# Performance work log

Measured on AMD Instinct MI355X. Metric: run time of the kernel, lower is better.

## Reference

```python
import jax, jax.numpy as jnp
import numpy as np

B, S, HID, NH = 2, 2048, 1024, 16
HD = HID // NH  # head_dim = 64


def setup_inputs() -> dict:
    key = jax.random.key(0)
    ks = jax.random.split(key, 11)
    sc = 1.0 / np.sqrt(HID)
    inp = {
        "query": jax.random.normal(ks[0], (B, S, HID), jnp.float32),
        "key_": jax.random.normal(ks[1], (B, S, HID), jnp.float32),
        "value": jax.random.normal(ks[2], (B, S, HID), jnp.float32),
        "Wq": jax.random.normal(ks[3], (HID, HID), jnp.float32) * sc,
        "bq": jnp.zeros((HID,), jnp.float32),
        "Wk": jax.random.normal(ks[4], (HID, HID), jnp.float32) * sc,
        "bk": jnp.zeros((HID,), jnp.float32),
        "Wv": jax.random.normal(ks[5], (HID, HID), jnp.float32) * sc,
        "bv": jnp.zeros((HID,), jnp.float32),
        "Wo": jax.random.normal(ks[6], (HID, HID), jnp.float32) * sc,
        "bo": jnp.zeros((HID,), jnp.float32),
    }
    return inp


def _split_heads(x):
    # [B, S, HID] -> [B, NH, S, HD]
    return x.reshape(B, S, NH, HD).transpose(0, 2, 1, 3)


def reference(query, key_, value, Wq, bq, Wk, bk, Wv, bv, Wo, bo):
    q = _split_heads(query @ Wq + bq)
    k = _split_heads(key_ @ Wk + bk)
    v = _split_heads(value @ Wv + bv)
    scale = 1.0 / jnp.sqrt(jnp.asarray(HD, q.dtype))
    # [B, NH, S, S] scores (unfused attention, as in the original module)
    scores = jnp.einsum("bhqd,bhkd->bhqk", q, k) * scale
    attn = jax.nn.softmax(scores, axis=-1)
    ctx = jnp.einsum("bhqk,bhkd->bhqd", attn, v)  # [B, NH, S, HD]
    ctx = ctx.transpose(0, 2, 1, 3).reshape(B, S, HID)
    return ctx @ Wo + bo
```

## Files before the change

kernel.cpp:

```cpp
#include <hip/hip_runtime.h>


typedef unsigned short u16;
typedef unsigned int u32;
typedef __bf16 bf16x8 __attribute__((ext_vector_type(8)));
typedef float f32x4 __attribute__((ext_vector_type(4)));
typedef u16 u16x4 __attribute__((ext_vector_type(4)));

__device__ __forceinline__ u16 f2bf(float f) {
  __bf16 h = (__bf16)f;
  return *(u16*)&h;
}

__device__ __forceinline__ void gll16(const void* g, void* l) {
  __builtin_amdgcn_global_load_lds(
      (const __attribute__((address_space(1))) u32*)g,
      (__attribute__((address_space(3))) u32*)l, 16, 0, 0);
}

__global__ __launch_bounds__(256) void prep_kernel(
    const float* __restrict__ q32, const float* __restrict__ k32,
    const float* __restrict__ v32,
    u16* __restrict__ qb, u16* __restrict__ kb, u16* __restrict__ vb,
    const float* __restrict__ W0, const float* __restrict__ W1,
    const float* __restrict__ W2, const float* __restrict__ W3,
    u16* __restrict__ T0, u16* __restrict__ T1,
    u16* __restrict__ T2, u16* __restrict__ T3) {
  int blk = blockIdx.x, tid = threadIdx.x;
  if (blk < 12288) {
    int which = blk >> 12;
    const float* in = (which == 0) ? q32 : (which == 1) ? k32 : v32;
    u16* out = (which == 0) ? qb : (which == 1) ? kb : vb;
    int i = (blk & 4095) * 256 + tid;
    float4 v = ((const float4*)in)[i];
    u16x4 o;
    o.x = f2bf(v.x); o.y = f2bf(v.y); o.z = f2bf(v.z); o.w = f2bf(v.w);
    ((u16x4*)out)[i] = o;
  } else {
    int tb = blk - 12288;
    int z = tb >> 10, rest = tb & 1023;
    const float* W = (z == 0) ? W0 : (z == 1) ? W1 : (z == 2) ? W2 : W3;
    u16* WT = (z == 0) ? T0 : (z == 1) ? T1 : (z == 2) ? T2 : T3;
    __shared__ float t[32][33];
    int bx = (rest & 31) * 32, by = (rest >> 5) * 32;
    int tx = tid & 31, ty = tid >> 5;
#pragma unroll
    for (int i = ty; i < 32; i += 8) t[i][tx] = W[(by + i) * 1024 + bx + tx];
    __syncthreads();
#pragma unroll
    for (int i = ty; i < 32; i += 8) WT[(bx + i) * 1024 + by + tx] = f2bf(t[tx][i]);
  }
}

struct GemmJob {
  const u16* A; const u16* BT; const float* bias;
  float* Cf; u16* Cb; int mode; float oscale;
};

template <int BN>
__global__ __launch_bounds__(256, 4) void gemm_sbuf(GemmJob j0, GemmJob j1, GemmJob j2) {
  constexpr int NT = BN / 32;
  constexpr int NBC = BN / 32;
  const int K = 1024, N = 1024;
  __shared__ __align__(16) u16 As[128 * 64];
  __shared__ __align__(16) u16 Bs[BN * 64];
  int blk = blockIdx.x, tid = threadIdx.x;
  int z, r0, bm, bn;
  if (BN == 128) {
    z = blk >> 8; r0 = blk & 255;
    int xcd = r0 & 7, i5 = r0 >> 3;
    bm = (xcd * 4 + (i5 & 3)) * 128;
    bn = (i5 >> 2) * 128;
  } else {
    z = 0; r0 = blk;
    int xcd = r0 & 7, i6 = r0 >> 3;
    bm = (xcd * 4 + (i6 & 3)) * 128;
    bn = (i6 >> 2) * 64;
  }
  GemmJob j = (z == 0) ? j0 : (z == 1) ? j1 : j2;
  int w = tid >> 6, lane = tid & 63, quad = lane >> 4, l16 = lane & 15;
  int wr = (w >> 1) * 64, wc = (w & 1) * (BN / 2);
  f32x4 acc[4][NT] = {};

  auto stage = [&](int kk) {
#pragma unroll
    for (int i = 0; i < 4; ++i) {
      int c = tid + i * 256;
      int r = c >> 3, jp = c & 7, jg = jp ^ (r & 7);
      gll16(&j.A[(size_t)(bm + r) * K + kk + jg * 8], &As[c * 8]);
    }
#pragma unroll
    for (int i = 0; i < NBC; ++i) {
      int c = tid + i * 256;
      int r = c >> 3, jp = c & 7, jg = jp ^ (r & 7);
      gll16(&j.BT[(size_t)(bn + r) * K + kk + jg * 8], &Bs[c * 8]);
    }
  };

  for (int it = 0; it < 16; ++it) {
    __syncthreads();
    stage(it * 64);
    __syncthreads();
#pragma unroll
    for (int ks = 0; ks < 2; ++ks) {
      bf16x8 af[4], bfr[NT];
#pragma unroll
      for (int mt = 0; mt < 4; ++mt) {
        int row = wr + mt * 16 + l16;
        af[mt] = *(const bf16x8*)&As[row * 64 + (((ks * 4 + quad) ^ (row & 7))) * 8];
      }
#pragma unroll
      for (int nt = 0; nt < NT; ++nt) {
        int row = wc + nt * 16 + l16;
        bfr[nt] = *(const bf16x8*)&Bs[row * 64 + (((ks * 4 + quad) ^ (row & 7))) * 8];
      }
#pragma unroll
      for (int mt = 0; mt < 4; ++mt)
#pragma unroll
        for (int nt = 0; nt < NT; ++nt)
          acc[mt][nt] = __builtin_amdgcn_mfma_f32_16x16x32_bf16(af[mt], bfr[nt], acc[mt][nt], 0, 0, 0);
    }
  }

#pragma unroll
  for (int mt = 0; mt < 4; ++mt)
#pragma unroll
    for (int nt = 0; nt < NT; ++nt)
#pragma unroll
      for (int r = 0; r < 4; ++r) {
        int row = bm + wr + mt * 16 + quad * 4 + r;
        int col = bn + wc + nt * 16 + l16;
        float v = (acc[mt][nt][r] + j.bias[col]) * j.oscale;
        if (j.mode == 0) {
          j.Cf[(size_t)row * N + col] = v;
        } else {
          int b = row >> 11, s = row & 2047, h = col >> 6, d = col & 63;
          u16 bv = f2bf(v);
          if (j.mode == 1)
            j.Cb[(((size_t)(b * 16 + h) * 2048 + s) << 6) + d] = bv;
          else
            j.Cb[((size_t)(b * 16 + h) * 64 + d) * 2048 + s] = bv;
        }
      }
}

__global__ __launch_bounds__(512) void attn_kernel(
    const u16* __restrict__ Q,
    const u16* __restrict__ Kk,
    const u16* __restrict__ VT,
    u16* __restrict__ ctx)
{
  __shared__ __align__(16) u16 Ks[128 * 64];
  __shared__ __align__(16) u16 Vs[64 * 128];
  __shared__ __align__(16) u16 PT[8 * 16 * 128];

  int blk = blockIdx.x;
  int qt = (blk >> 3) & 15;
  int bh = (blk & 7) * 4 + (blk >> 7);
  int b = bh >> 4, h = bh & 15;
  const u16* Qb = Q + ((size_t)bh * 2048 + qt * 128) * 64;
  const u16* Kb = Kk + (size_t)bh * 2048 * 64;
  const u16* Vb = VT + (size_t)bh * 64 * 2048;
  int tid = threadIdx.x, w = tid >> 6, lane = tid & 63, quad = lane >> 4, l16 = lane & 15;
  int rowbase = w * 16;
  u16* PTw = &PT[w * 16 * 128];

  bf16x8 qf[2];
#pragma unroll
  for (int ks = 0; ks < 2; ++ks)
    qf[ks] = *(const bf16x8*)&Qb[(rowbase + l16) * 64 + ks * 32 + quad * 8];

  f32x4 Oacc[4] = {};
  float lacc = 0.f;

  for (int kv = 0; kv < 16; ++kv) {
    int kbase = kv * 128;
    __syncthreads();
#pragma unroll
    for (int i = 0; i < 2; ++i) {
      int c = tid + i * 512;
      int r = c >> 3, jp = c & 7, jg = jp ^ (r & 7);
      gll16(&Kb[(size_t)(kbase + r) * 64 + jg * 8], &Ks[c * 8]);
    }
#pragma unroll
    for (int i = 0; i < 2; ++i) {
      int c = tid + i * 512;
      int d = c >> 4, jp = c & 15, jg = jp ^ (d & 15);
      gll16(&Vb[(size_t)d * 2048 + kbase + jg * 8], &Vs[c * 8]);
    }
    __syncthreads();

    f32x4 Sacc[8] = {};
#pragma unroll
    for (int nt = 0; nt < 8; ++nt) {
      int r = nt * 16 + l16;
#pragma unroll
      for (int ks = 0; ks < 2; ++ks) {
        bf16x8 kfr = *(const bf16x8*)&Ks[r * 64 + ((ks * 4 + quad) ^ (l16 & 7)) * 8];
        Sacc[nt] = __builtin_amdgcn_mfma_f32_16x16x32_bf16(kfr, qf[ks], Sacc[nt], 0, 0, 0);
      }
    }

#pragma unroll
    for (int nt = 0; nt < 8; ++nt) {
      u16x4 pk;
#pragma unroll
      for (int r = 0; r < 4; ++r) {
        float p = exp2f(Sacc[nt][r]);
        lacc += p;
        pk[r] = f2bf(p);
      }
      int jj = nt * 2 + (quad >> 1);
      *(u16x4*)&PTw[l16 * 128 + ((jj ^ l16) * 8) + (quad & 1) * 4] = pk;
    }

#pragma unroll
    for (int ks2 = 0; ks2 < 4; ++ks2) {
      bf16x8 pfB = *(const bf16x8*)&PTw[l16 * 128 + (((ks2 * 4 + quad) ^ l16)) * 8];
#pragma unroll
      for (int dt = 0; dt < 4; ++dt) {
        int d = dt * 16 + l16;
        bf16x8 vf = *(const bf16x8*)&Vs[d * 128 + (((ks2 * 4 + quad) ^ l16)) * 8];
        Oacc[dt] = __builtin_amdgcn_mfma_f32_16x16x32_bf16(vf, pfB, Oacc[dt], 0, 0, 0);
      }
    }
  }

  float l = lacc;
  l += __shfl_xor(l, 16, 64);
  l += __shfl_xor(l, 32, 64);
  float linv = 1.0f / l;

  int s = qt * 128 + rowbase + l16;
#pragma unroll
  for (int dt = 0; dt < 4; ++dt) {
    u16x4 o;
#pragma unroll
    for (int r = 0; r < 4; ++r) o[r] = f2bf(Oacc[dt][r] * linv);
    *(u16x4*)&ctx[(size_t)(b * 2048 + s) * 1024 + h * 64 + dt * 16 + quad * 4] = o;
  }
}


extern "C" void kernel_launch(void* const* d_in, const int* in_sizes, int n_in,
                              void* d_out, int out_size, void* d_ws, size_t ws_size,
                              hipStream_t stream) {
  const float* query = (const float*)d_in[0];
  const float* key_  = (const float*)d_in[1];
  const float* value = (const float*)d_in[2];
  const float* Wq = (const float*)d_in[3];
  const float* bq = (const float*)d_in[4];
  const float* Wk = (const float*)d_in[5];
  const float* bk = (const float*)d_in[6];
  const float* Wv = (const float*)d_in[7];
  const float* bv = (const float*)d_in[8];
  const float* Wo = (const float*)d_in[9];
  const float* bo = (const float*)d_in[10];
  float* out = (float*)d_out;

  char* ws = (char*)d_ws;
  const size_t MB = 1024 * 1024;
  u16* Aq  = (u16*)(ws + 0 * MB);
  u16* Ak  = (u16*)(ws + 8 * MB);
  u16* Av  = (u16*)(ws + 16 * MB);
  u16* WqT = (u16*)(ws + 24 * MB);
  u16* WkT = (u16*)(ws + 26 * MB);
  u16* WvT = (u16*)(ws + 28 * MB);
  u16* WoT = (u16*)(ws + 30 * MB);
  u16* Qp  = (u16*)(ws + 32 * MB);
  u16* Kp  = (u16*)(ws + 40 * MB);
  u16* VTp = (u16*)(ws + 48 * MB);
  u16* Ctx = (u16*)(ws + 56 * MB);

  prep_kernel<<<16384, 256, 0, stream>>>(query, key_, value, Aq, Ak, Av,
                                         Wq, Wk, Wv, Wo, WqT, WkT, WvT, WoT);

  const float sc = 0.125f * 1.44269504f;
  GemmJob jq{Aq, WqT, bq, nullptr, Qp, 1, sc};
  GemmJob jk{Ak, WkT, bk, nullptr, Kp, 1, 1.0f};
  GemmJob jv{Av, WvT, bv, nullptr, VTp, 2, 1.0f};
  gemm_sbuf<128><<<768, 256, 0, stream>>>(jq, jk, jv);

  attn_kernel<<<512, 512, 0, stream>>>(Qp, Kp, VTp, Ctx);

  GemmJob jo{Ctx, WoT, bo, out, nullptr, 0, 1.0f};
  gemm_sbuf<64><<<512, 256, 0, stream>>>(jo, jo, jo);
}
```

Baseline: 248.2 us.

## Double-buffer K/V tiles and interleave QK, softmax, PV in 32-key chunks

Adds a second LDS buffer for K and V so the next tile's global-to-LDS loads are issued before computing on the current tile, leaving one barrier per iteration instead of two. The S/P/PV work is split into four 32-key chunks, which shrinks the per-wave P scratch and lowers score register pressure. s_setprio is raised around the MFMA groups to favour matrix issue. The cost is double the K/V LDS footprint, which may reduce occupancy. There is also a possible hazard: the loads issued into the other buffer are not waited on before the barrier, so correctness depends on the barrier's implicit vmcnt wait.

```diff
diff --git a/kernel.cpp b/kernel.cpp
--- a/kernel.cpp
+++ b/kernel.cpp
@@ -150,9 +150,9 @@
     const u16* __restrict__ VT,
     u16* __restrict__ ctx)
 {
-  __shared__ __align__(16) u16 Ks[128 * 64];
-  __shared__ __align__(16) u16 Vs[64 * 128];
-  __shared__ __align__(16) u16 PT[8 * 16 * 128];
+  __shared__ __align__(16) u16 Ks[2][128 * 64];
+  __shared__ __align__(16) u16 Vs[2][64 * 128];
+  __shared__ __align__(16) u16 PT[8 * 16 * 32];
 
   int blk = blockIdx.x;
   int qt = (blk >> 3) & 15;
@@ -163,7 +163,7 @@
   const u16* Vb = VT + (size_t)bh * 64 * 2048;
   int tid = threadIdx.x, w = tid >> 6, lane = tid & 63, quad = lane >> 4, l16 = lane & 15;
   int rowbase = w * 16;
-  u16* PTw = &PT[w * 16 * 128];
+  u16* PTw = &PT[w * 16 * 32];
 
   bf16x8 qf[2];
 #pragma unroll
@@ -173,57 +173,69 @@
   f32x4 Oacc[4] = {};
   float lacc = 0.f;
 
-  for (int kv = 0; kv < 16; ++kv) {
-    int kbase = kv * 128;
-    __syncthreads();
+  auto stage = [&](int t, int sel) {
+    int kbase = t * 128;
 #pragma unroll
     for (int i = 0; i < 2; ++i) {
       int c = tid + i * 512;
       int r = c >> 3, jp = c & 7, jg = jp ^ (r & 7);
-      gll16(&Kb[(size_t)(kbase + r) * 64 + jg * 8], &Ks[c * 8]);
+      gll16(&Kb[(size_t)(kbase + r) * 64 + jg * 8], &Ks[sel][c * 8]);
     }
 #pragma unroll
     for (int i = 0; i < 2; ++i) {
       int c = tid + i * 512;
       int d = c >> 4, jp = c & 15, jg = jp ^ (d & 15);
-      gll16(&Vb[(size_t)d * 2048 + kbase + jg * 8], &Vs[c * 8]);
-    }
-    __syncthreads();
-
-    f32x4 Sacc[8] = {};
-#pragma unroll
-    for (int nt = 0; nt < 8; ++nt) {
-      int r = nt * 16 + l16;
-#pragma unroll
-      for (int ks = 0; ks < 2; ++ks) {
-        bf16x8 kfr = *(const bf16x8*)&Ks[r * 64 + ((ks * 4 + quad) ^ (l16 & 7)) * 8];
-        Sacc[nt] = __builtin_amdgcn_mfma_f32_16x16x32_bf16(kfr, qf[ks], Sacc[nt], 0, 0, 0);
-      }
-    }
-
-#pragma unroll
-    for (int nt = 0; nt < 8; ++nt) {
-      u16x4 pk;
-#pragma unroll
-      for (int r = 0; r < 4; ++r) {
-        float p = exp2f(Sacc[nt][r]);
-        lacc += p;
-        pk[r] = f2bf(p);
-      }
-      int jj = nt * 2 + (quad >> 1);
-      *(u16x4*)&PTw[l16 * 128 + ((jj ^ l16) * 8) + (quad & 1) * 4] = pk;
-    }
-
-#pragma unroll
-    for (int ks2 = 0; ks2 < 4; ++ks2) {
-      bf16x8 pfB = *(const bf16x8*)&PTw[l16 * 128 + (((ks2 * 4 + quad) ^ l16)) * 8];
+      gll16(&Vb[(size_t)d * 2048 + kbase + jg * 8], &Vs[sel][c * 8]);
+    }
+  };
+
+  stage(0, 0);
+  __syncthreads();
+
+  for (int kv = 0; kv < 16; ++kv) {
+    int cur = kv & 1;
+    if (kv < 15) stage(kv + 1, cur ^ 1);
+
+#pragma unroll
+    for (int c = 0; c < 4; ++c) {
+      f32x4 Sc[2] = {};
+      __builtin_amdgcn_s_setprio(1);
+#pragma unroll
+      for (int nt2 = 0; nt2 < 2; ++nt2) {
+        int r = (c * 2 + nt2) * 16 + l16;
+#pragma unroll
+        for (int ks = 0; ks < 2; ++ks) {
+          bf16x8 kfr = *(const bf16x8*)&Ks[cur][r * 64 + ((ks * 4 + quad) ^ (l16 & 7)) * 8];
+          Sc[nt2] = __builtin_amdgcn_mfma_f32_16x16x32_bf16(kfr, qf[ks], Sc[nt2], 0, 0, 0);
+        }
+      }
+      __builtin_amdgcn_s_setprio(0);
+
+#pragma unroll
+      for (int nt2 = 0; nt2 < 2; ++nt2) {
+        u16x4 pk;
+#pragma unroll
+        for (int r = 0; r < 4; ++r) {
+          float p = exp2f(Sc[nt2][r]);
+          lacc += p;
+          pk[r] = f2bf(p);
+        }
+        int jl = nt2 * 2 + (quad >> 1);
+        *(u16x4*)&PTw[l16 * 32 + ((jl ^ (l16 & 3)) * 8) + (quad & 1) * 4] = pk;
+      }
+
+      bf16x8 pfB = *(const bf16x8*)&PTw[l16 * 32 + ((quad ^ (l16 & 3)) * 8)];
+      __builtin_amdgcn_s_setprio(1);
 #pragma unroll
       for (int dt = 0; dt < 4; ++dt) {
         int d = dt * 16 + l16;
-        bf16x8 vf = *(const bf16x8*)&Vs[d * 128 + (((ks2 * 4 + quad) ^ l16)) * 8];
+        bf16x8 vf = *(const bf16x8*)&Vs[cur][d * 128 + (((c * 4 + quad) ^ l16)) * 8];
         Oacc[dt] = __builtin_amdgcn_mfma_f32_16x16x32_bf16(vf, pfB, Oacc[dt], 0, 0, 0);
       }
-    }
+      __builtin_amdgcn_s_setprio(0);
+    }
+
+    __syncthreads();
   }
 
   float l = lacc;
```

Result: no change. 245.8 us (-1.0%).
